# Optimization experiments

Hardware: AMD Instinct MI355X
Metric: run time of the kernel (lower is better)

Reference implementation:

```python
import jax, jax.numpy as jnp
import numpy as np

OUT_F = 4096
IN_F = 4096
GROUP = 128
NUM_GROUPS = IN_F // GROUP  # 32
PACKED = (OUT_F * IN_F + 3) // 4  # 4194304


def setup_inputs() -> dict:
    key = jax.random.key(0)
    k1, k2, k3, k4, k5 = jax.random.split(key, 5)
    x = jax.random.normal(k1, (4, 2048, IN_F), dtype=jnp.float32)
    weight_packed = jax.random.randint(k2, (PACKED,), 0, 256, dtype=jnp.int32)
    scales = jax.random.uniform(k3, (OUT_F, NUM_GROUPS), dtype=jnp.float32)
    zeros = jax.random.normal(k4, (OUT_F, NUM_GROUPS), dtype=jnp.float32)
    bias = jax.random.normal(k5, (OUT_F,), dtype=jnp.float32)
    return {"x": x, "weight_packed": weight_packed, "scales": scales,
            "zeros": zeros, "bias": bias}


def _dequant_weight(weight_packed, scales, zeros, dtype):
    shifts = jnp.array([0, 2, 4, 6], dtype=jnp.int32)
    w_int = (weight_packed[:, None] >> shifts[None, :]) & 3  # [PACKED, 4]
    w_int = w_int.reshape(-1)[: OUT_F * IN_F].reshape(OUT_F, NUM_GROUPS, GROUP)
    # Per-group dequant: w = q * scale + zero
    w = w_int.astype(dtype) * scales[:, :, None] + zeros[:, :, None]
    return w.reshape(OUT_F, IN_F)


def reference(x, weight_packed, scales, zeros, bias):
    w = _dequant_weight(weight_packed, scales, zeros, x.dtype)  # [out, in]
    # F.linear: x @ w.T + bias
    out = jnp.einsum('bsi,oi->bso', x, w) + bias
    return out
```

## Files before the change

kernel.cpp:

```cpp
#include <hip/hip_runtime.h>
#include <hip/hip_bf16.h>
#include <cstdint>
#include <cstddef>

#define KDIM 4096
#define NDIM 4096

typedef __attribute__((ext_vector_type(8))) short short8;
typedef __attribute__((ext_vector_type(8))) __bf16 bf16x8;
typedef __attribute__((ext_vector_type(4))) float f32x4;

__device__ __forceinline__ unsigned short bf16_rne(float f) {
    unsigned int u = __builtin_bit_cast(unsigned int, f);
    u += 0x7fffu + ((u >> 16) & 1u);
    return (unsigned short)(u >> 16);
}

__device__ __forceinline__ void gload_lds16(const unsigned short* g, unsigned short* l) {
    __builtin_amdgcn_global_load_lds(
        (const __attribute__((address_space(1))) unsigned int*)g,
        (__attribute__((address_space(3))) unsigned int*)l,
        16, 0, 0);
}

__global__ void cvt_x_kernel(const float* __restrict__ x, unsigned short* __restrict__ xb) {
    long i = (long)blockIdx.x * blockDim.x + threadIdx.x;
    float4 a = ((const float4*)x)[2 * i];
    float4 b = ((const float4*)x)[2 * i + 1];
    union { unsigned short u[8]; short8 v; } r;
    r.u[0] = bf16_rne(a.x); r.u[1] = bf16_rne(a.y);
    r.u[2] = bf16_rne(a.z); r.u[3] = bf16_rne(a.w);
    r.u[4] = bf16_rne(b.x); r.u[5] = bf16_rne(b.y);
    r.u[6] = bf16_rne(b.z); r.u[7] = bf16_rne(b.w);
    ((short8*)xb)[i] = r.v;
}

__global__ void dequant_w_kernel(const int* __restrict__ wp,
                                 const float* __restrict__ scales,
                                 const float* __restrict__ zeros,
                                 unsigned short* __restrict__ wb) {
    long i = (long)blockIdx.x * blockDim.x + threadIdx.x;
    int2 p = ((const int2*)wp)[i];
    long base = i * 8;
    int o = (int)(base >> 12);
    int g = (int)((base & 4095) >> 7);
    float s = scales[o * 32 + g];
    float z = zeros[o * 32 + g];
    union { unsigned short u[8]; short8 v; } r;
#pragma unroll
    for (int j = 0; j < 4; ++j) {
        r.u[j]     = bf16_rne((float)((p.x >> (2 * j)) & 3) * s + z);
        r.u[4 + j] = bf16_rne((float)((p.y >> (2 * j)) & 3) * s + z);
    }
    ((short8*)wb)[i] = r.v;
}


#define PH_SYNC_MFMA \
    __builtin_amdgcn_s_barrier(); \
    asm volatile("s_waitcnt lgkmcnt(0)" ::: "memory"); \
    __builtin_amdgcn_sched_barrier(0); \
    __builtin_amdgcn_s_setprio(1);

#define PH_END \
    __builtin_amdgcn_s_setprio(0); \
    __builtin_amdgcn_s_barrier();

#define VMCNT4 \
    __builtin_amdgcn_sched_barrier(0); \
    asm volatile("s_waitcnt vmcnt(4)" ::: "memory"); \
    __builtin_amdgcn_sched_barrier(0);

#define RD_A(arr, DOFF, mh) \
    _Pragma("unroll") \
    for (int mi_ = 0; mi_ < 4; ++mi_) { \
        arr[mi_][0] = *(const short8*)&sm[(DOFF) + aBase + ((mh)*4 + mi_) * 1024 + sw0]; \
        arr[mi_][1] = *(const short8*)&sm[(DOFF) + aBase + ((mh)*4 + mi_) * 1024 + sw1]; \
    }

#define RD_B(DOFF, n0) \
    _Pragma("unroll") \
    for (int ni_ = 0; ni_ < 2; ++ni_) { \
        bF[(n0) + ni_][0] = *(const short8*)&sm[(DOFF) + bBase + ((n0) + ni_) * 1024 + sw0]; \
        bF[(n0) + ni_][1] = *(const short8*)&sm[(DOFF) + bBase + ((n0) + ni_) * 1024 + sw1]; \
    }

#define QUAD(af, mh, nh) \
    _Pragma("unroll") \
    for (int s_ = 0; s_ < 2; ++s_) { \
      _Pragma("unroll") \
      for (int mi_ = 0; mi_ < 4; ++mi_) { \
        _Pragma("unroll") \
        for (int ni_ = 0; ni_ < 2; ++ni_) { \
          acc[(mh)*4+mi_][(nh)*2+ni_] = __builtin_amdgcn_mfma_f32_16x16x32_bf16( \
            __builtin_bit_cast(bf16x8, af[mi_][s_]), \
            __builtin_bit_cast(bf16x8, bF[(nh)*2+ni_][s_]), \
            acc[(mh)*4+mi_][(nh)*2+ni_], 0, 0, 0); \
        } } }

__global__ __launch_bounds__(512, 2) void gemm256(const unsigned short* __restrict__ A,
                                                  const unsigned short* __restrict__ B,
                                                  const float* __restrict__ bias,
                                                  float* __restrict__ C) {
    __shared__ __align__(16) unsigned short sm[65536];

    const int tid = threadIdx.x;
    const int w64 = tid >> 6;
    const int lane = tid & 63;

    const int nwg = gridDim.x;
    const int chunk = nwg >> 3;
    const int s_id = (blockIdx.x & 7) * chunk + (blockIdx.x >> 3);
    const int nm = nwg >> 4;
    const int bm = s_id % nm;
    const int bn = s_id / nm;
    const int row0 = bm * 256;
    const int col0 = bn * 256;

    const int wr = w64 >> 2;
    const int wc = w64 & 3;

    const int srow = tid >> 3;
    const int swzk = 8 * ((tid & 7) ^ ((tid >> 3) & 7));
    const unsigned short* srcA = A + (size_t)(row0 + srow) * KDIM + swzk;
    const unsigned short* srcB = B + (size_t)(col0 + srow) * KDIM + swzk;

    const int lr = lane & 15;
    const int lk4 = lane >> 4;
    const int l7 = lane & 7;
    const int sw0 = 8 * (((0 << 2) + lk4) ^ l7);
    const int sw1 = 8 * (((1 << 2) + lk4) ^ l7);
    const int aBase = (wr * 128 + lr) * 64;
    const int bBase = 16384 + (wc * 64 + lr) * 64;

    f32x4 acc[8][4] = {};
    short8 aF[4][2], aG[4][2], bF[4][2];

    auto stageA = [&](int hh, int tile, int db) {
        const unsigned short* g = srcA + (size_t)hh * 128 * KDIM + (size_t)tile * 64;
        unsigned short* l = &sm[db * 32768 + hh * 8192 + w64 * 512];
        gload_lds16(g, l);
        gload_lds16(g + (size_t)64 * KDIM, l + 4096);
    };
    auto stageB = [&](int hh, int tile, int db) {
        const unsigned short* g = srcB + (size_t)hh * 128 * KDIM + (size_t)tile * 64;
        unsigned short* l = &sm[db * 32768 + 16384 + hh * 8192 + w64 * 512];
        gload_lds16(g, l);
        gload_lds16(g + (size_t)64 * KDIM, l + 4096);
    };

    const int NT = KDIM / 64;

    stageB(0, 0, 0); stageB(1, 0, 0); stageA(0, 0, 0); stageA(1, 0, 0);
    stageB(0, 1, 1); stageB(1, 1, 1);
    VMCNT4
    __builtin_amdgcn_s_barrier();

    for (int i = 0; i < NT / 2; ++i) {
        const int e = 2 * i;
        const int o = e + 1;
        const int e2 = (e + 2 < NT) ? e + 2 : e;
        const int o2 = (o + 2 < NT) ? o + 2 : o;

        RD_A(aF, 0, 0)
        RD_B(0, 0)
        stageA(0, o, 1);
        PH_SYNC_MFMA
        QUAD(aF, 0, 0)
        PH_END
        RD_B(0, 2)
        stageA(1, o, 1);
        PH_SYNC_MFMA
        QUAD(aF, 0, 1)
        PH_END
        RD_A(aG, 0, 1)
        stageB(0, e2, 0);
        PH_SYNC_MFMA
        QUAD(aG, 1, 0)
        PH_END
        stageB(1, e2, 0);
        VMCNT4
        PH_SYNC_MFMA
        QUAD(aG, 1, 1)
        PH_END

        RD_A(aF, 32768, 0)
        RD_B(32768, 0)
        stageA(0, e2, 0);
        PH_SYNC_MFMA
        QUAD(aF, 0, 0)
        PH_END
        RD_B(32768, 2)
        stageA(1, e2, 0);
        PH_SYNC_MFMA
        QUAD(aF, 0, 1)
        PH_END
        RD_A(aG, 32768, 1)
        stageB(0, o2, 1);
        PH_SYNC_MFMA
        QUAD(aG, 1, 0)
        PH_END
        stageB(1, o2, 1);
        VMCNT4
        PH_SYNC_MFMA
        QUAD(aG, 1, 1)
        PH_END
    }

    __builtin_amdgcn_sched_barrier(0);
    asm volatile("s_waitcnt vmcnt(0)" ::: "memory");
    __builtin_amdgcn_sched_barrier(0);

#pragma unroll
    for (int m = 0; m < 8; ++m) {
#pragma unroll
        for (int n = 0; n < 4; ++n) {
            int col = col0 + wc * 64 + n * 16 + lr;
            float bz = bias[col];
#pragma unroll
            for (int r = 0; r < 4; ++r) {
                int row = row0 + wr * 128 + m * 16 + lk4 * 4 + r;
                C[(size_t)row * NDIM + col] = acc[m][n][r] + bz;
            }
        }
    }
}

__global__ void fallback_kernel(const float* __restrict__ x, const int* __restrict__ wp,
                                const float* __restrict__ scales, const float* __restrict__ zeros,
                                const float* __restrict__ bias, float* __restrict__ out) {
    int o = blockIdx.x * 256 + threadIdx.x;
    int m = blockIdx.y;
    __shared__ float xs[KDIM];
    for (int i = threadIdx.x; i < KDIM; i += 256) xs[i] = x[(size_t)m * KDIM + i];
    __syncthreads();
    float acc = 0.f;
    for (int g = 0; g < 32; ++g) {
        float s = scales[o * 32 + g], z = zeros[o * 32 + g];
        float aq = 0.f, ax = 0.f;
        for (int j = 0; j < 32; ++j) {
            int p = wp[o * 1024 + g * 32 + j];
            int kb = g * 128 + j * 4;
#pragma unroll
            for (int q = 0; q < 4; ++q) {
                float xv = xs[kb + q];
                aq += xv * (float)((p >> (2 * q)) & 3);
                ax += xv;
            }
        }
        acc += s * aq + z * ax;
    }
    out[(size_t)m * NDIM + o] = acc + bias[o];
}

extern "C" void kernel_launch(void* const* d_in, const int* in_sizes, int n_in,
                              void* d_out, int out_size, void* d_ws, size_t ws_size,
                              hipStream_t stream) {
    const float* x      = (const float*)d_in[0];
    const int*   wp     = (const int*)d_in[1];
    const float* scales = (const float*)d_in[2];
    const float* zeros  = (const float*)d_in[3];
    const float* bias   = (const float*)d_in[4];
    float* out = (float*)d_out;

    const long M = (long)in_sizes[0] / KDIM;
    const long PACKED = (long)in_sizes[1];
    const size_t need = (size_t)M * KDIM * 2 + (size_t)NDIM * KDIM * 2;

    if (ws_size >= need && (M % 256) == 0) {
        unsigned short* xb = (unsigned short*)d_ws;
        unsigned short* wb = xb + (size_t)M * KDIM;
        cvt_x_kernel<<<(M * KDIM / 8) / 256, 256, 0, stream>>>(x, xb);
        dequant_w_kernel<<<(PACKED / 2) / 256, 256, 0, stream>>>(wp, scales, zeros, wb);
        int nwg = (int)(M / 256) * (NDIM / 256);
        gemm256<<<nwg, 512, 0, stream>>>(xb, wb, bias, out);
    } else {
        dim3 grid(NDIM / 256, M);
        fallback_kernel<<<grid, 256, 0, stream>>>(x, wp, scales, zeros, bias, out);
    }
}
```

Baseline: 286.1 us.

## Software-pipeline LDS fragment reads one phase ahead of MFMA clusters

Each phase's LDS fragment reads now issue right after the barrier and wait, ahead of the MFMA block that uses the previous fragments. B fragments are split into two ping-pong buffers so loads for the next quad can overlap the current quad's MFMAs. A prologue preloads the first fragments, and the epilogue now also waits on lgkmcnt. This is meant to hide LDS read latency behind matrix math, at the cost of more complex ordering and possible register pressure or hazards around buffer reuse.

```diff
diff --git a/kernel.cpp b/kernel.cpp
--- a/kernel.cpp
+++ b/kernel.cpp
@@ -56,9 +56,12 @@
 }
 
 
-#define PH_SYNC_MFMA \
+#define PH_BAR_WAIT \
     __builtin_amdgcn_s_barrier(); \
     asm volatile("s_waitcnt lgkmcnt(0)" ::: "memory"); \
+    __builtin_amdgcn_sched_barrier(0);
+
+#define PH_MFMA_BEGIN \
     __builtin_amdgcn_sched_barrier(0); \
     __builtin_amdgcn_s_setprio(1);
 
@@ -78,14 +81,14 @@
         arr[mi_][1] = *(const short8*)&sm[(DOFF) + aBase + ((mh)*4 + mi_) * 1024 + sw1]; \
     }
 
-#define RD_B(DOFF, n0) \
+#define RD_B(bx, DOFF, n0) \
     _Pragma("unroll") \
     for (int ni_ = 0; ni_ < 2; ++ni_) { \
-        bF[(n0) + ni_][0] = *(const short8*)&sm[(DOFF) + bBase + ((n0) + ni_) * 1024 + sw0]; \
-        bF[(n0) + ni_][1] = *(const short8*)&sm[(DOFF) + bBase + ((n0) + ni_) * 1024 + sw1]; \
-    }
-
-#define QUAD(af, mh, nh) \
+        bx[ni_][0] = *(const short8*)&sm[(DOFF) + bBase + ((n0) + ni_) * 1024 + sw0]; \
+        bx[ni_][1] = *(const short8*)&sm[(DOFF) + bBase + ((n0) + ni_) * 1024 + sw1]; \
+    }
+
+#define QUADX(af, bx, mh, nh) \
     _Pragma("unroll") \
     for (int s_ = 0; s_ < 2; ++s_) { \
       _Pragma("unroll") \
@@ -94,7 +97,7 @@
         for (int ni_ = 0; ni_ < 2; ++ni_) { \
           acc[(mh)*4+mi_][(nh)*2+ni_] = __builtin_amdgcn_mfma_f32_16x16x32_bf16( \
             __builtin_bit_cast(bf16x8, af[mi_][s_]), \
-            __builtin_bit_cast(bf16x8, bF[(nh)*2+ni_][s_]), \
+            __builtin_bit_cast(bf16x8, bx[ni_][s_]), \
             acc[(mh)*4+mi_][(nh)*2+ni_], 0, 0, 0); \
         } } }
 
@@ -134,7 +137,7 @@
     const int bBase = 16384 + (wc * 64 + lr) * 64;
 
     f32x4 acc[8][4] = {};
-    short8 aF[4][2], aG[4][2], bF[4][2];
+    short8 aF[4][2], aG[4][2], bQ0[2][2], bQ1[2][2];
 
     auto stageA = [&](int hh, int tile, int db) {
         const unsigned short* g = srcA + (size_t)hh * 128 * KDIM + (size_t)tile * 64;
@@ -155,6 +158,9 @@
     stageB(0, 1, 1); stageB(1, 1, 1);
     VMCNT4
     __builtin_amdgcn_s_barrier();
+    RD_A(aF, 0, 0)
+    RD_B(bQ0, 0, 0)
+    __builtin_amdgcn_sched_barrier(0);
 
     for (int i = 0; i < NT / 2; ++i) {
         const int e = 2 * i;
@@ -162,53 +168,61 @@
         const int e2 = (e + 2 < NT) ? e + 2 : e;
         const int o2 = (o + 2 < NT) ? o + 2 : o;
 
-        RD_A(aF, 0, 0)
-        RD_B(0, 0)
         stageA(0, o, 1);
-        PH_SYNC_MFMA
-        QUAD(aF, 0, 0)
-        PH_END
-        RD_B(0, 2)
+        PH_BAR_WAIT
+        RD_B(bQ1, 0, 2)
+        PH_MFMA_BEGIN
+        QUADX(aF, bQ0, 0, 0)
+        PH_END
         stageA(1, o, 1);
-        PH_SYNC_MFMA
-        QUAD(aF, 0, 1)
-        PH_END
+        PH_BAR_WAIT
         RD_A(aG, 0, 1)
+        PH_MFMA_BEGIN
+        QUADX(aF, bQ1, 0, 1)
+        PH_END
         stageB(0, e2, 0);
-        PH_SYNC_MFMA
-        QUAD(aG, 1, 0)
+        PH_BAR_WAIT
+        PH_MFMA_BEGIN
+        QUADX(aG, bQ0, 1, 0)
         PH_END
         stageB(1, e2, 0);
         VMCNT4
-        PH_SYNC_MFMA
-        QUAD(aG, 1, 1)
-        PH_END
-
+        PH_BAR_WAIT
         RD_A(aF, 32768, 0)
-        RD_B(32768, 0)
+        RD_B(bQ0, 32768, 0)
+        PH_MFMA_BEGIN
+        QUADX(aG, bQ1, 1, 1)
+        PH_END
+
         stageA(0, e2, 0);
-        PH_SYNC_MFMA
-        QUAD(aF, 0, 0)
-        PH_END
-        RD_B(32768, 2)
+        PH_BAR_WAIT
+        RD_B(bQ1, 32768, 2)
+        PH_MFMA_BEGIN
+        QUADX(aF, bQ0, 0, 0)
+        PH_END
         stageA(1, e2, 0);
-        PH_SYNC_MFMA
-        QUAD(aF, 0, 1)
-        PH_END
+        PH_BAR_WAIT
         RD_A(aG, 32768, 1)
+        PH_MFMA_BEGIN
+        QUADX(aF, bQ1, 0, 1)
+        PH_END
         stageB(0, o2, 1);
-        PH_SYNC_MFMA
-        QUAD(aG, 1, 0)
+        PH_BAR_WAIT
+        PH_MFMA_BEGIN
+        QUADX(aG, bQ0, 1, 0)
         PH_END
         stageB(1, o2, 1);
         VMCNT4
-        PH_SYNC_MFMA
-        QUAD(aG, 1, 1)
-        PH_END
-    }
-
-    __builtin_amdgcn_sched_barrier(0);
-    asm volatile("s_waitcnt vmcnt(0)" ::: "memory");
+        PH_BAR_WAIT
+        RD_A(aF, 0, 0)
+        RD_B(bQ0, 0, 0)
+        PH_MFMA_BEGIN
+        QUADX(aG, bQ1, 1, 1)
+        PH_END
+    }
+
+    __builtin_amdgcn_sched_barrier(0);
+    asm volatile("s_waitcnt vmcnt(0) lgkmcnt(0)" ::: "memory");
     __builtin_amdgcn_sched_barrier(0);
 
 #pragma unroll
```

Measured after the change: 554.0 us. +93.6%, slower.
